# Optimization experiments

Measured on AMD Instinct MI355X. Metric: run time of the kernel, lower is better.

The kernel has to match this reference:

```python
import jax, jax.numpy as jnp
import numpy as np

N = 50000       # num nodes
E = 800000      # num edges (avg degree 16)
D = 128         # in_dim = hidden_dim = out_dim
C = 10          # n_classes
NOISE_STD = 0.1
LN_EPS = 1e-5


def layer_norm(x, g, b):
    mu = jnp.mean(x, axis=-1, keepdims=True)
    var = jnp.mean((x - mu) ** 2, axis=-1, keepdims=True)
    return (x - mu) * jax.lax.rsqrt(var + LN_EPS) * g + b


def gcn_conv(x, W, b, src, dst, dout_isqrt, din_isqrt):
    # DGL GraphConv, norm='both': h = D_in^{-1/2} A (D_out^{-1/2} x W) + b
    h = (x * dout_isqrt[:, None]) @ W              # [N, D] transform first (in>=out)
    agg = jax.ops.segment_sum(h[src], dst, num_segments=x.shape[0])  # SpMM via gather+scatter
    return agg * din_isqrt[:, None] + b


def setup_inputs() -> dict:
    key = jax.random.key(0)
    ks = jax.random.split(key, 16)
    inv = 1.0 / np.sqrt(D)
    return {
        "feat": jax.random.normal(ks[0], (N, D), jnp.float32),
        "noise": jax.random.normal(ks[1], (N, D), jnp.float32),
        "node_mask": jax.random.bernoulli(ks[2], 0.1, (N,)),
        "src": jax.random.randint(ks[3], (E,), 0, N, jnp.int32),
        "dst": jax.random.randint(ks[4], (E,), 0, N, jnp.int32),
        "mask_token": jax.random.normal(ks[5], (D,), jnp.float32) * inv,
        "W0": jax.random.normal(ks[6], (D, D), jnp.float32) * inv,
        "b0": jnp.zeros((D,), jnp.float32),
        "ln0_g": jnp.ones((D,), jnp.float32),
        "ln0_b": jnp.zeros((D,), jnp.float32),
        "W1": jax.random.normal(ks[7], (D, D), jnp.float32) * inv,
        "b1": jnp.zeros((D,), jnp.float32),
        "ln1_g": jnp.ones((D,), jnp.float32),
        "ln1_b": jnp.zeros((D,), jnp.float32),
        "dec_W1": jax.random.normal(ks[8], (D, D), jnp.float32) * inv,
        "dec_b1": jnp.zeros((D,), jnp.float32),
        "dec_W2": jax.random.normal(ks[9], (D, D), jnp.float32) * inv,
        "dec_b2": jnp.zeros((D,), jnp.float32),
        "cls_W": jax.random.normal(ks[10], (D, C), jnp.float32) * inv,
        "cls_b": jnp.zeros((C,), jnp.float32),
    }


def reference(feat, noise, node_mask, src, dst, mask_token,
              W0, b0, ln0_g, ln0_b, W1, b1, ln1_g, ln1_b,
              dec_W1, dec_b1, dec_W2, dec_b2, cls_W, cls_b):
    n = feat.shape[0]
    ones_e = jnp.ones(src.shape, feat.dtype)
    deg_out = jax.ops.segment_sum(ones_e, src, num_segments=n)
    deg_in = jax.ops.segment_sum(ones_e, dst, num_segments=n)
    dout_isqrt = jnp.where(deg_out > 0, jax.lax.rsqrt(jnp.maximum(deg_out, 1.0)), 0.0)
    din_isqrt = jnp.where(deg_in > 0, jax.lax.rsqrt(jnp.maximum(deg_in, 1.0)), 0.0)

    # node masking + noise injection (eval mode: dropout is identity)
    x_masked = jnp.where(node_mask[:, None], mask_token[None, :], feat) + noise * NOISE_STD

    # encoder: layer 0 (conv -> LN -> ReLU), layer 1 (conv -> LN)
    h = gcn_conv(x_masked, W0, b0, src, dst, dout_isqrt, din_isqrt)
    h = jax.nn.relu(layer_norm(h, ln0_g, ln0_b))
    h = gcn_conv(h, W1, b1, src, dst, dout_isqrt, din_isqrt)
    z = layer_norm(h, ln1_g, ln1_b)

    x_recon = jax.nn.relu(z @ dec_W1 + dec_b1) @ dec_W2 + dec_b2
    logits = z @ cls_W + cls_b
    return (x_recon, feat, node_mask, z, logits)
```

## Files before the change

### kernel.cpp

```cpp
#include <hip/hip_runtime.h>
#include <hip/hip_bf16.h>

#define LN_EPS 1e-5f
#define HB 64
#define HSEG 12800
#define NBLK 128
#define BROWS 64
#define WPSTRIDE 17408

typedef __attribute__((ext_vector_type(8))) short short8;
typedef __attribute__((ext_vector_type(4))) float f32x4;

__device__ __forceinline__ unsigned short f2bf(float f) {
    unsigned int u = __float_as_uint(f);
    u += 0x7fffu + ((u >> 16) & 1u);
    return (unsigned short)(u >> 16);
}
__device__ __forceinline__ unsigned int pack2bf(float a, float b) {
    return (unsigned int)f2bf(a) | ((unsigned int)f2bf(b) << 16);
}
__device__ __forceinline__ float bflo(unsigned int v) { return __uint_as_float(v << 16); }
__device__ __forceinline__ float bfhi(unsigned int v) { return __uint_as_float(v & 0xffff0000u); }

__global__ __launch_bounds__(512) void k_hist(const int* __restrict__ src, int* __restrict__ partials,
                                              int N, int E) {
    __shared__ int h[HSEG];
    int chunk = blockIdx.x & (HB - 1);
    int seg = blockIdx.x >> 6;
    int lo = seg * HSEG;
    int len = N - lo;
    if (len > HSEG) len = HSEG;
    if (len <= 0) return;
    for (int i = threadIdx.x; i < len; i += 512) h[i] = 0;
    __syncthreads();
    int per = (E + HB - 1) / HB;
    int e0 = chunk * per, e1 = min(e0 + per, E);
    for (int e = e0 + threadIdx.x; e < e1; e += 512) {
        int s = src[e] - lo;
        if ((unsigned)s < (unsigned)len) atomicAdd(&h[s], 1);
    }
    __syncthreads();
    for (int i = threadIdx.x; i < len; i += 512)
        partials[(size_t)chunk * N + lo + i] = h[i];
}

__global__ __launch_bounds__(256) void k_reduce(const int* __restrict__ partials,
                                                float* __restrict__ doutv, int N) {
    int i = blockIdx.x * 256 + threadIdx.x;
    if (i >= N) return;
    int s = 0;
#pragma unroll
    for (int b = 0; b < HB; ++b) s += partials[(size_t)b * N + i];
    doutv[i] = s > 0 ? 1.0f / sqrtf((float)s) : 0.0f;
}

__global__ __launch_bounds__(256) void k_front(const int* __restrict__ dst, int* __restrict__ counts,
                                               const float* __restrict__ Wa, const float* __restrict__ Wb,
                                               const float* __restrict__ Wc, const float* __restrict__ Wd,
                                               unsigned short* __restrict__ wpack,
                                               const float* __restrict__ feat, const float* __restrict__ noise,
                                               const int* __restrict__ mask, const float* __restrict__ token,
                                               unsigned short* __restrict__ xs, float* __restrict__ feat_out,
                                               float* __restrict__ mask_out,
                                               int nbuck, int E, int n) {
    __shared__ int h[1024];
    int bid = blockIdx.x;
    int tid = threadIdx.x;
    if (bid < NBLK) {
        for (int i = tid; i < nbuck; i += 256) h[i] = 0;
        __syncthreads();
        int per = (E + NBLK - 1) / NBLK;
        int e0 = bid * per, e1 = min(e0 + per, E);
        for (int e = e0 + tid; e < e1; e += 256) atomicAdd(&h[dst[e] >> 6], 1);
        __syncthreads();
        for (int i = tid; i < nbuck; i += 256) counts[(size_t)i * NBLK + bid] = h[i];
        return;
    }
    bid -= NBLK;
    if (bid < 256) {
        int idx = bid * 256 + tid;
        int wsel = idx >> 14;
        int within = idx & 16383;
        const float* W = wsel == 0 ? Wa : wsel == 1 ? Wb : wsel == 2 ? Wc : Wd;
        int c = within >> 7, kk = within & 127;
        wpack[(size_t)wsel * WPSTRIDE + c * 136 + kk] = f2bf(W[kk * 128 + c]);
        return;
    }
    bid -= 256;
    int i = bid * 256 + tid;
    int total = n * 32;
    if (i >= total) return;
    int row = i >> 5, q = i & 31;
    float4 f = ((const float4*)feat)[i];
    float4 nz = ((const float4*)noise)[i];
    bool m = mask[row] != 0;
    float4 b = f;
    if (m) b = ((const float4*)token)[q];
    uint2 p;
    p.x = pack2bf(b.x + 0.1f * nz.x, b.y + 0.1f * nz.y);
    p.y = pack2bf(b.z + 0.1f * nz.z, b.w + 0.1f * nz.w);
    ((uint2*)xs)[i] = p;
    ((float4*)feat_out)[i] = f;
    if (q == 0) mask_out[row] = m ? 1.0f : 0.0f;
}

__global__ __launch_bounds__(128) void k_binB1(const int* __restrict__ counts, int* __restrict__ tot) {
    __shared__ int sm[128];
    int t = threadIdx.x;
    sm[t] = counts[(size_t)blockIdx.x * NBLK + t];
    __syncthreads();
#pragma unroll
    for (int o = 64; o >= 1; o >>= 1) {
        if (t < o) sm[t] += sm[t + o];
        __syncthreads();
    }
    if (t == 0) tot[blockIdx.x] = sm[0];
}

__global__ __launch_bounds__(1024) void k_binB2(const int* __restrict__ tot, int* __restrict__ base,
                                                int nbuck, int E) {
    __shared__ int sm[1024];
    int t = threadIdx.x;
    int v = (t < nbuck) ? tot[t] : 0;
    sm[t] = v;
    __syncthreads();
    for (int o = 1; o < 1024; o <<= 1) {
        int u = (t >= o) ? sm[t - o] : 0;
        __syncthreads();
        sm[t] += u;
        __syncthreads();
    }
    if (t < nbuck) base[t] = sm[t] - v;
    if (t == 0) base[nbuck] = E;
}

__global__ __launch_bounds__(128) void k_binB3(const int* __restrict__ counts, const int* __restrict__ base,
                                               int* __restrict__ offs) {
    __shared__ int sm[128];
    int t = threadIdx.x;
    int v = counts[(size_t)blockIdx.x * NBLK + t];
    sm[t] = v;
    __syncthreads();
    for (int o = 1; o < 128; o <<= 1) {
        int u = (t >= o) ? sm[t - o] : 0;
        __syncthreads();
        sm[t] += u;
        __syncthreads();
    }
    offs[(size_t)blockIdx.x * NBLK + t] = base[blockIdx.x] + sm[t] - v;
}

__global__ __launch_bounds__(256) void k_binC(const int* __restrict__ src, const int* __restrict__ dst,
                                              const int* __restrict__ offs, uint2* __restrict__ binned,
                                              int nbuck, int E) {
    __shared__ int cur[1024];
    for (int i = threadIdx.x; i < nbuck; i += 256) cur[i] = offs[(size_t)i * NBLK + blockIdx.x];
    __syncthreads();
    int per = (E + NBLK - 1) / NBLK;
    int e0 = blockIdx.x * per, e1 = min(e0 + per, E);
    for (int e = e0 + threadIdx.x; e < e1; e += 256) {
        int d = dst[e];
        int p = atomicAdd(&cur[d >> 6], 1);
        binned[p] = make_uint2((unsigned)src[e], (unsigned)d);
    }
}

__global__ __launch_bounds__(256) void k_csr(const uint2* __restrict__ binned, const int* __restrict__ base,
                                             int* __restrict__ row_ptr, int* __restrict__ csr_src, int N) {
    __shared__ int hcnt[BROWS], ccur[BROWS];
    int b = blockIdx.x, t = threadIdx.x;
    int e0 = base[b], e1 = base[b + 1];
    if (t < BROWS) hcnt[t] = 0;
    __syncthreads();
    for (int e = e0 + t; e < e1; e += 256)
        atomicAdd(&hcnt[binned[e].y & (BROWS - 1)], 1);
    __syncthreads();
    if (t < BROWS) {
        int acc = 0;
        for (int r = 0; r < t; ++r) acc += hcnt[r];
        ccur[t] = acc;
        int gw = b * BROWS + t;
        if (gw <= N) row_ptr[gw] = e0 + acc;
    }
    __syncthreads();
    for (int e = e0 + t; e < e1; e += 256) {
        uint2 ed = binned[e];
        int p = atomicAdd(&ccur[ed.y & (BROWS - 1)], 1);
        csr_src[e0 + p] = (int)ed.x;
    }
}

template <int EPI, int OUT_BF16, int DOUT>
__global__ __launch_bounds__(256) void k_gemm_mfma(const unsigned short* __restrict__ A,
                                                   const unsigned short* __restrict__ Wp,
                                                   const float* __restrict__ bias,
                                                   const float* __restrict__ dscale,
                                                   void* __restrict__ Cout, int n) {
    __shared__ uint4 BtV[2176];
    unsigned short* Bt = (unsigned short*)BtV;
    int tid = threadIdx.x;
    const uint4* Wv = (const uint4*)Wp;
    for (int i = tid; i < 2176; i += 256) BtV[i] = Wv[i];
    __syncthreads();

    int wid = tid >> 6, lane = tid & 63;
    int q = lane >> 4, m = lane & 15;
    int r0 = blockIdx.x * 128 + wid * 32;

    f32x4 acc[2][8];
#pragma unroll
    for (int i = 0; i < 2; ++i)
#pragma unroll
        for (int j = 0; j < 8; ++j) acc[i][j] = (f32x4){0.f, 0.f, 0.f, 0.f};

#pragma unroll
    for (int ks = 0; ks < 4; ++ks) {
        int k0 = ks * 32 + q * 8;
        short8 a[2];
#pragma unroll
        for (int i = 0; i < 2; ++i) {
            int row = r0 + i * 16 + m;
            if (row > n - 1) row = n - 1;
            a[i] = *(const short8*)(A + (size_t)row * 128 + k0);
        }
        short8 b[8];
#pragma unroll
        for (int j = 0; j < 8; ++j)
            b[j] = *(const short8*)(&Bt[(j * 16 + m) * 136 + k0]);
#pragma unroll
        for (int i = 0; i < 2; ++i)
#pragma unroll
            for (int j = 0; j < 8; ++j)
                acc[i][j] = __builtin_amdgcn_mfma_f32_16x16x32_bf16(a[i], b[j], acc[i][j], 0, 0, 0);
    }

    float bv[8];
    if (EPI >= 1) {
#pragma unroll
        for (int j = 0; j < 8; ++j) bv[j] = bias[j * 16 + m];
    }

#pragma unroll
    for (int i = 0; i < 2; ++i) {
#pragma unroll
        for (int r = 0; r < 4; ++r) {
            int row = r0 + i * 16 + q * 4 + r;
            if (row < n) {
                float ds = DOUT ? dscale[row] : 1.0f;
#pragma unroll
                for (int j = 0; j < 8; ++j) {
                    float v = acc[i][j][r];
                    if (DOUT) v *= ds;
                    if (EPI >= 1) v += bv[j];
                    if (EPI == 2) v = fmaxf(v, 0.0f);
                    if (OUT_BF16)
                        ((unsigned short*)Cout)[(size_t)row * 128 + j * 16 + m] = f2bf(v);
                    else
                        ((float*)Cout)[(size_t)row * 128 + j * 16 + m] = v;
                }
            }
        }
    }
}

__global__ __launch_bounds__(256) void k_gemm_cls(const unsigned short* __restrict__ A,
                                                  const unsigned short* __restrict__ Wp,
                                                  const float* __restrict__ bias,
                                                  void* __restrict__ Cout,
                                                  const float* __restrict__ cW, const float* __restrict__ cbias,
                                                  float* __restrict__ logits,
                                                  int n, int C, int gb) {
    __shared__ uint4 BtV[2176];
    unsigned short* Bt = (unsigned short*)BtV;
    int tid = threadIdx.x;
    if ((int)blockIdx.x >= gb) {
        int gpos = ((int)blockIdx.x - gb) * 256 + tid;
        int row = gpos >> 4, c = gpos & 15;
        if (row >= n || c >= C) return;
        const unsigned int* zr = (const unsigned int*)(A + (size_t)row * 128);
        float acc = cbias[c];
#pragma unroll 8
        for (int kk = 0; kk < 64; ++kk) {
            unsigned int v = zr[kk];
            acc = fmaf(bflo(v), cW[(2 * kk) * C + c], acc);
            acc = fmaf(bfhi(v), cW[(2 * kk + 1) * C + c], acc);
        }
        logits[(size_t)row * C + c] = acc;
        return;
    }
    const uint4* Wv = (const uint4*)Wp;
    for (int i = tid; i < 2176; i += 256) BtV[i] = Wv[i];
    __syncthreads();

    int wid = tid >> 6, lane = tid & 63;
    int q = lane >> 4, m = lane & 15;
    int r0 = blockIdx.x * 128 + wid * 32;

    f32x4 acc[2][8];
#pragma unroll
    for (int i = 0; i < 2; ++i)
#pragma unroll
        for (int j = 0; j < 8; ++j) acc[i][j] = (f32x4){0.f, 0.f, 0.f, 0.f};

#pragma unroll
    for (int ks = 0; ks < 4; ++ks) {
        int k0 = ks * 32 + q * 8;
        short8 a[2];
#pragma unroll
        for (int i = 0; i < 2; ++i) {
            int row = r0 + i * 16 + m;
            if (row > n - 1) row = n - 1;
            a[i] = *(const short8*)(A + (size_t)row * 128 + k0);
        }
        short8 b[8];
#pragma unroll
        for (int j = 0; j < 8; ++j)
            b[j] = *(const short8*)(&Bt[(j * 16 + m) * 136 + k0]);
#pragma unroll
        for (int i = 0; i < 2; ++i)
#pragma unroll
            for (int j = 0; j < 8; ++j)
                acc[i][j] = __builtin_amdgcn_mfma_f32_16x16x32_bf16(a[i], b[j], acc[i][j], 0, 0, 0);
    }

    float bv[8];
#pragma unroll
    for (int j = 0; j < 8; ++j) bv[j] = bias[j * 16 + m];

#pragma unroll
    for (int i = 0; i < 2; ++i) {
#pragma unroll
        for (int r = 0; r < 4; ++r) {
            int row = r0 + i * 16 + q * 4 + r;
            if (row < n) {
#pragma unroll
                for (int j = 0; j < 8; ++j) {
                    float v = acc[i][j][r] + bv[j];
                    v = fmaxf(v, 0.0f);
                    ((unsigned short*)Cout)[(size_t)row * 128 + j * 16 + m] = f2bf(v);
                }
            }
        }
    }
}

template <int MODE>
__global__ __launch_bounds__(256) void k_agg_ln(const unsigned short* __restrict__ H,
                                                const int* __restrict__ row_ptr,
                                                const int* __restrict__ csr_src,
                                                const float* __restrict__ cb, const float* __restrict__ g,
                                                const float* __restrict__ bt,
                                                float* __restrict__ out_f32, unsigned short* __restrict__ out_bf,
                                                int n) {
    int gw = (blockIdx.x * blockDim.x + threadIdx.x) >> 6;
    int lane = threadIdx.x & 63;
    if (gw >= n) return;
    int beg = row_ptr[gw], end = row_ptr[gw + 1];
    int cnt = end - beg;
    const unsigned int* Hu = (const unsigned int*)H;
    float ax0 = 0.f, ay0 = 0.f, ax1 = 0.f, ay1 = 0.f;
    float ax2 = 0.f, ay2 = 0.f, ax3 = 0.f, ay3 = 0.f;
    for (int c0 = beg; c0 < end; c0 += 64) {
        int m = end - c0;
        if (m > 64) m = 64;
        int myidx = (lane < m) ? csr_src[c0 + lane] : 0;
        int k = 0;
        for (; k + 7 < m; k += 8) {
            int s0 = __shfl(myidx, k + 0), s1 = __shfl(myidx, k + 1);
            int s2 = __shfl(myidx, k + 2), s3 = __shfl(myidx, k + 3);
            int s4 = __shfl(myidx, k + 4), s5 = __shfl(myidx, k + 5);
            int s6 = __shfl(myidx, k + 6), s7 = __shfl(myidx, k + 7);
            unsigned int v0 = Hu[(size_t)s0 * 64 + lane];
            unsigned int v1 = Hu[(size_t)s1 * 64 + lane];
            unsigned int v2 = Hu[(size_t)s2 * 64 + lane];
            unsigned int v3 = Hu[(size_t)s3 * 64 + lane];
            unsigned int v4 = Hu[(size_t)s4 * 64 + lane];
            unsigned int v5 = Hu[(size_t)s5 * 64 + lane];
            unsigned int v6 = Hu[(size_t)s6 * 64 + lane];
            unsigned int v7 = Hu[(size_t)s7 * 64 + lane];
            ax0 += bflo(v0); ay0 += bfhi(v0);
            ax1 += bflo(v1); ay1 += bfhi(v1);
            ax2 += bflo(v2); ay2 += bfhi(v2);
            ax3 += bflo(v3); ay3 += bfhi(v3);
            ax0 += bflo(v4); ay0 += bfhi(v4);
            ax1 += bflo(v5); ay1 += bfhi(v5);
            ax2 += bflo(v6); ay2 += bfhi(v6);
            ax3 += bflo(v7); ay3 += bfhi(v7);
        }
        for (; k < m; ++k) {
            int s0 = __shfl(myidx, k);
            unsigned int v0 = Hu[(size_t)s0 * 64 + lane];
            ax0 += bflo(v0); ay0 += bfhi(v0);
        }
    }
    int d0 = lane * 2;
    float sc = cnt > 0 ? 1.0f / sqrtf((float)cnt) : 0.0f;
    float2 cbv = *(const float2*)(cb + d0);
    float2 x;
    x.x = (ax0 + ax1 + ax2 + ax3) * sc + cbv.x;
    x.y = (ay0 + ay1 + ay2 + ay3) * sc + cbv.y;

    float s = x.x + x.y;
#pragma unroll
    for (int mm = 32; mm >= 1; mm >>= 1) s += __shfl_xor(s, mm, 64);
    float mu = s * (1.0f / 128.0f);
    float dx = x.x - mu, dy = x.y - mu;
    float v = dx * dx + dy * dy;
#pragma unroll
    for (int mm = 32; mm >= 1; mm >>= 1) v += __shfl_xor(v, mm, 64);
    float inv = 1.0f / sqrtf(v * (1.0f / 128.0f) + LN_EPS);
    float2 gv = *(const float2*)(g + d0);
    float2 bv = *(const float2*)(bt + d0);
    float y0 = dx * inv * gv.x + bv.x;
    float y1 = dy * inv * gv.y + bv.y;
    if (MODE == 1) {
        y0 = fmaxf(y0, 0.0f);
        y1 = fmaxf(y1, 0.0f);
    } else {
        *(float2*)(out_f32 + (size_t)gw * 128 + d0) = make_float2(y0, y1);
    }
    ((unsigned int*)out_bf)[(size_t)gw * 64 + lane] = pack2bf(y0, y1);
}

extern "C" void kernel_launch(void* const* d_in, const int* in_sizes, int n_in,
                              void* d_out, int out_size, void* d_ws, size_t ws_size,
                              hipStream_t stream) {
    const float* feat  = (const float*)d_in[0];
    const float* noise = (const float*)d_in[1];
    const int*   nmask = (const int*)d_in[2];
    const int*   src   = (const int*)d_in[3];
    const int*   dst   = (const int*)d_in[4];
    const float* token = (const float*)d_in[5];
    const float* W0    = (const float*)d_in[6];
    const float* b0    = (const float*)d_in[7];
    const float* ln0g  = (const float*)d_in[8];
    const float* ln0b  = (const float*)d_in[9];
    const float* W1    = (const float*)d_in[10];
    const float* b1    = (const float*)d_in[11];
    const float* ln1g  = (const float*)d_in[12];
    const float* ln1b  = (const float*)d_in[13];
    const float* dW1   = (const float*)d_in[14];
    const float* db1   = (const float*)d_in[15];
    const float* dW2   = (const float*)d_in[16];
    const float* db2   = (const float*)d_in[17];
    const float* cW    = (const float*)d_in[18];
    const float* cbias = (const float*)d_in[19];

    const int N = in_sizes[0] / 128;
    const int E = in_sizes[3];
    const int C = in_sizes[19];
    const size_t ND = (size_t)N * 128;
    const int NBUCK = (N + BROWS - 1) / BROWS;
    const int NSEG = (N + HSEG - 1) / HSEG;

    float* out       = (float*)d_out;
    float* out_recon = out;
    float* out_feat  = out + ND;
    float* out_mask  = out + 2 * ND;
    float* out_z     = out + 2 * ND + N;
    float* out_log   = out + 3 * ND + N;

    char* w = (char*)d_ws;
    unsigned short* bufX = (unsigned short*)w; w += ND * 2;
    unsigned short* bufH = (unsigned short*)w; w += ND * 2;
    unsigned short* zbf  = (unsigned short*)w; w += ND * 2;
    unsigned short* wpack = (unsigned short*)w; w += (size_t)4 * WPSTRIDE * 2;
    float* doutv   = (float*)w; w += (size_t)N * 4;
    int* row_ptr   = (int*)w;   w += (size_t)(N + 4) * 4;
    int* csr_src   = (int*)w;   w += (size_t)E * 4;
    int* scratch   = (int*)w;

    int* partials = scratch;
    uint2* binned = (uint2*)scratch;
    int* counts = scratch + (size_t)HB * N;
    int* tot    = counts + (size_t)NBUCK * NBLK;
    int* base   = tot + NBUCK;
    int* offs   = base + NBUCK + 2;

    k_hist<<<HB * NSEG, 512, 0, stream>>>(src, partials, N, E);

    int prep_blocks = (N * 32 + 255) / 256;
    k_front<<<NBLK + 256 + prep_blocks, 256, 0, stream>>>(dst, counts, W0, W1, dW1, dW2, wpack,
                                                          feat, noise, nmask, token,
                                                          bufX, out_feat, out_mask, NBUCK, E, N);

    int nb = (N + 255) / 256;
    k_reduce<<<nb, 256, 0, stream>>>(partials, doutv, N);
    k_binB1<<<NBUCK, 128, 0, stream>>>(counts, tot);
    k_binB2<<<1, 1024, 0, stream>>>(tot, base, NBUCK, E);
    k_binB3<<<NBUCK, 128, 0, stream>>>(counts, base, offs);

    k_binC<<<NBLK, 256, 0, stream>>>(src, dst, offs, binned, NBUCK, E);
    k_csr<<<NBUCK, 256, 0, stream>>>(binned, base, row_ptr, csr_src, N);

    int gb = (N + 127) / 128;
    int rb = (N * 64 + 255) / 256;

    k_gemm_mfma<0, 1, 1><<<gb, 256, 0, stream>>>(bufX, wpack + 0 * WPSTRIDE, nullptr, doutv, bufH, N);
    k_agg_ln<1><<<rb, 256, 0, stream>>>(bufH, row_ptr, csr_src, b0, ln0g, ln0b, nullptr, bufX, N);

    k_gemm_mfma<0, 1, 1><<<gb, 256, 0, stream>>>(bufX, wpack + 1 * WPSTRIDE, nullptr, doutv, bufH, N);
    k_agg_ln<0><<<rb, 256, 0, stream>>>(bufH, row_ptr, csr_src, b1, ln1g, ln1b, out_z, zbf, N);

    int cls_blocks = (N * 16 + 255) / 256;
    k_gemm_cls<<<gb + cls_blocks, 256, 0, stream>>>(zbf, wpack + 2 * WPSTRIDE, db1, bufX,
                                                    cW, cbias, out_log, N, C, gb);

    k_gemm_mfma<1, 0, 0><<<gb, 256, 0, stream>>>(bufX, wpack + 3 * WPSTRIDE, db2, nullptr, out_recon, N);
}
```

Measured before the change: 212.1 us.

## Fuse decoder GEMMs via LDS and split edge gather across half-waves

The two decoder GEMMs become one kernel: the ReLU'd hidden tile is staged in LDS as bf16 and fed straight into the second MFMA GEMM, so the intermediate no longer goes through global memory. The classifier head moves to its own kernel. The aggregation kernel now has each half-wave gather a different neighbor row with 8-byte loads and combines the halves with a cross-half shuffle, which doubles the edges in flight per wave. The costs are doubled LDS per decoder block, which may lower occupancy, and the extra shuffle reduction step.

```diff
diff --git a/kernel.cpp b/kernel.cpp
--- a/kernel.cpp
+++ b/kernel.cpp
@@ -263,34 +263,19 @@
     }
 }
 
-__global__ __launch_bounds__(256) void k_gemm_cls(const unsigned short* __restrict__ A,
-                                                  const unsigned short* __restrict__ Wp,
-                                                  const float* __restrict__ bias,
-                                                  void* __restrict__ Cout,
-                                                  const float* __restrict__ cW, const float* __restrict__ cbias,
-                                                  float* __restrict__ logits,
-                                                  int n, int C, int gb) {
-    __shared__ uint4 BtV[2176];
-    unsigned short* Bt = (unsigned short*)BtV;
+__global__ __launch_bounds__(256) void k_dec(const unsigned short* __restrict__ A,
+                                             const unsigned short* __restrict__ Wp1, const float* __restrict__ bias1,
+                                             const unsigned short* __restrict__ Wp2, const float* __restrict__ bias2,
+                                             float* __restrict__ Cout, int n) {
+    __shared__ uint4 W1V[2176];
+    __shared__ uint4 W2V[2176];
     int tid = threadIdx.x;
-    if ((int)blockIdx.x >= gb) {
-        int gpos = ((int)blockIdx.x - gb) * 256 + tid;
-        int row = gpos >> 4, c = gpos & 15;
-        if (row >= n || c >= C) return;
-        const unsigned int* zr = (const unsigned int*)(A + (size_t)row * 128);
-        float acc = cbias[c];
-#pragma unroll 8
-        for (int kk = 0; kk < 64; ++kk) {
-            unsigned int v = zr[kk];
-            acc = fmaf(bflo(v), cW[(2 * kk) * C + c], acc);
-            acc = fmaf(bfhi(v), cW[(2 * kk + 1) * C + c], acc);
-        }
-        logits[(size_t)row * C + c] = acc;
-        return;
-    }
-    const uint4* Wv = (const uint4*)Wp;
-    for (int i = tid; i < 2176; i += 256) BtV[i] = Wv[i];
-    __syncthreads();
+    const uint4* w1 = (const uint4*)Wp1;
+    const uint4* w2 = (const uint4*)Wp2;
+    for (int i = tid; i < 2176; i += 256) { W1V[i] = w1[i]; W2V[i] = w2[i]; }
+    __syncthreads();
+    unsigned short* W1s = (unsigned short*)W1V;
+    unsigned short* W2s = (unsigned short*)W2V;
 
     int wid = tid >> 6, lane = tid & 63;
     int q = lane >> 4, m = lane & 15;
@@ -301,7 +286,6 @@
     for (int i = 0; i < 2; ++i)
 #pragma unroll
         for (int j = 0; j < 8; ++j) acc[i][j] = (f32x4){0.f, 0.f, 0.f, 0.f};
-
 #pragma unroll
     for (int ks = 0; ks < 4; ++ks) {
         int k0 = ks * 32 + q * 8;
@@ -315,33 +299,66 @@
         short8 b[8];
 #pragma unroll
         for (int j = 0; j < 8; ++j)
-            b[j] = *(const short8*)(&Bt[(j * 16 + m) * 136 + k0]);
+            b[j] = *(const short8*)(&W1s[(j * 16 + m) * 136 + k0]);
 #pragma unroll
         for (int i = 0; i < 2; ++i)
 #pragma unroll
             for (int j = 0; j < 8; ++j)
                 acc[i][j] = __builtin_amdgcn_mfma_f32_16x16x32_bf16(a[i], b[j], acc[i][j], 0, 0, 0);
     }
-
     float bv[8];
 #pragma unroll
-    for (int j = 0; j < 8; ++j) bv[j] = bias[j * 16 + m];
-
-#pragma unroll
-    for (int i = 0; i < 2; ++i) {
+    for (int j = 0; j < 8; ++j) bv[j] = bias1[j * 16 + m];
+
+    __syncthreads();
+    unsigned short* T = W1s;
+#pragma unroll
+    for (int i = 0; i < 2; ++i)
+#pragma unroll
+        for (int r = 0; r < 4; ++r) {
+            int lrow = wid * 32 + i * 16 + q * 4 + r;
+#pragma unroll
+            for (int j = 0; j < 8; ++j) {
+                float v = acc[i][j][r] + bv[j];
+                T[lrow * 136 + j * 16 + m] = f2bf(fmaxf(v, 0.0f));
+            }
+        }
+    __syncthreads();
+
+#pragma unroll
+    for (int i = 0; i < 2; ++i)
+#pragma unroll
+        for (int j = 0; j < 8; ++j) acc[i][j] = (f32x4){0.f, 0.f, 0.f, 0.f};
+#pragma unroll
+    for (int ks = 0; ks < 4; ++ks) {
+        int k0 = ks * 32 + q * 8;
+        short8 a[2];
+#pragma unroll
+        for (int i = 0; i < 2; ++i)
+            a[i] = *(const short8*)(&T[(wid * 32 + i * 16 + m) * 136 + k0]);
+        short8 b[8];
+#pragma unroll
+        for (int j = 0; j < 8; ++j)
+            b[j] = *(const short8*)(&W2s[(j * 16 + m) * 136 + k0]);
+#pragma unroll
+        for (int i = 0; i < 2; ++i)
+#pragma unroll
+            for (int j = 0; j < 8; ++j)
+                acc[i][j] = __builtin_amdgcn_mfma_f32_16x16x32_bf16(a[i], b[j], acc[i][j], 0, 0, 0);
+    }
+#pragma unroll
+    for (int j = 0; j < 8; ++j) bv[j] = bias2[j * 16 + m];
+#pragma unroll
+    for (int i = 0; i < 2; ++i)
 #pragma unroll
         for (int r = 0; r < 4; ++r) {
             int row = r0 + i * 16 + q * 4 + r;
             if (row < n) {
 #pragma unroll
-                for (int j = 0; j < 8; ++j) {
-                    float v = acc[i][j][r] + bv[j];
-                    v = fmaxf(v, 0.0f);
-                    ((unsigned short*)Cout)[(size_t)row * 128 + j * 16 + m] = f2bf(v);
-                }
-            }
-        }
-    }
+                for (int j = 0; j < 8; ++j)
+                    Cout[(size_t)row * 128 + j * 16 + m] = acc[i][j][r] + bv[j];
+            }
+        }
 }
 
 template <int MODE>
@@ -357,69 +374,110 @@
     if (gw >= n) return;
     int beg = row_ptr[gw], end = row_ptr[gw + 1];
     int cnt = end - beg;
-    const unsigned int* Hu = (const unsigned int*)H;
-    float ax0 = 0.f, ay0 = 0.f, ax1 = 0.f, ay1 = 0.f;
-    float ax2 = 0.f, ay2 = 0.f, ax3 = 0.f, ay3 = 0.f;
+    const uint2* H2 = (const uint2*)H;
+    int half = lane >> 5;
+    int hl = lane & 31;
+    float a0 = 0.f, a1 = 0.f, a2 = 0.f, a3 = 0.f;
     for (int c0 = beg; c0 < end; c0 += 64) {
         int m = end - c0;
         if (m > 64) m = 64;
         int myidx = (lane < m) ? csr_src[c0 + lane] : 0;
         int k = 0;
+        for (; k + 15 < m; k += 16) {
+            uint2 v[8];
+#pragma unroll
+            for (int p = 0; p < 8; ++p) {
+                int s = __shfl(myidx, k + 2 * p + half);
+                v[p] = H2[(size_t)s * 32 + hl];
+            }
+#pragma unroll
+            for (int p = 0; p < 8; ++p) {
+                a0 += bflo(v[p].x); a1 += bfhi(v[p].x);
+                a2 += bflo(v[p].y); a3 += bfhi(v[p].y);
+            }
+        }
         for (; k + 7 < m; k += 8) {
-            int s0 = __shfl(myidx, k + 0), s1 = __shfl(myidx, k + 1);
-            int s2 = __shfl(myidx, k + 2), s3 = __shfl(myidx, k + 3);
-            int s4 = __shfl(myidx, k + 4), s5 = __shfl(myidx, k + 5);
-            int s6 = __shfl(myidx, k + 6), s7 = __shfl(myidx, k + 7);
-            unsigned int v0 = Hu[(size_t)s0 * 64 + lane];
-            unsigned int v1 = Hu[(size_t)s1 * 64 + lane];
-            unsigned int v2 = Hu[(size_t)s2 * 64 + lane];
-            unsigned int v3 = Hu[(size_t)s3 * 64 + lane];
-            unsigned int v4 = Hu[(size_t)s4 * 64 + lane];
-            unsigned int v5 = Hu[(size_t)s5 * 64 + lane];
-            unsigned int v6 = Hu[(size_t)s6 * 64 + lane];
-            unsigned int v7 = Hu[(size_t)s7 * 64 + lane];
-            ax0 += bflo(v0); ay0 += bfhi(v0);
-            ax1 += bflo(v1); ay1 += bfhi(v1);
-            ax2 += bflo(v2); ay2 += bfhi(v2);
-            ax3 += bflo(v3); ay3 += bfhi(v3);
-            ax0 += bflo(v4); ay0 += bfhi(v4);
-            ax1 += bflo(v5); ay1 += bfhi(v5);
-            ax2 += bflo(v6); ay2 += bfhi(v6);
-            ax3 += bflo(v7); ay3 += bfhi(v7);
-        }
-        for (; k < m; ++k) {
-            int s0 = __shfl(myidx, k);
-            unsigned int v0 = Hu[(size_t)s0 * 64 + lane];
-            ax0 += bflo(v0); ay0 += bfhi(v0);
-        }
-    }
-    int d0 = lane * 2;
+            uint2 v[4];
+#pragma unroll
+            for (int p = 0; p < 4; ++p) {
+                int s = __shfl(myidx, k + 2 * p + half);
+                v[p] = H2[(size_t)s * 32 + hl];
+            }
+#pragma unroll
+            for (int p = 0; p < 4; ++p) {
+                a0 += bflo(v[p].x); a1 += bfhi(v[p].x);
+                a2 += bflo(v[p].y); a3 += bfhi(v[p].y);
+            }
+        }
+        for (; k < m; k += 2) {
+            int e = k + half;
+            int s = __shfl(myidx, (e < m) ? e : k);
+            uint2 vv = H2[(size_t)s * 32 + hl];
+            if (e < m) {
+                a0 += bflo(vv.x); a1 += bfhi(vv.x);
+                a2 += bflo(vv.y); a3 += bfhi(vv.y);
+            }
+        }
+    }
+    a0 += __shfl_xor(a0, 32, 64);
+    a1 += __shfl_xor(a1, 32, 64);
+    a2 += __shfl_xor(a2, 32, 64);
+    a3 += __shfl_xor(a3, 32, 64);
+
+    int d0 = hl * 4;
     float sc = cnt > 0 ? 1.0f / sqrtf((float)cnt) : 0.0f;
-    float2 cbv = *(const float2*)(cb + d0);
-    float2 x;
-    x.x = (ax0 + ax1 + ax2 + ax3) * sc + cbv.x;
-    x.y = (ay0 + ay1 + ay2 + ay3) * sc + cbv.y;
-
-    float s = x.x + x.y;
-#pragma unroll
-    for (int mm = 32; mm >= 1; mm >>= 1) s += __shfl_xor(s, mm, 64);
+    float4 cbv = *(const float4*)(cb + d0);
+    float x0 = a0 * sc + cbv.x;
+    float x1 = a1 * sc + cbv.y;
+    float x2 = a2 * sc + cbv.z;
+    float x3 = a3 * sc + cbv.w;
+
+    float s = x0 + x1 + x2 + x3;
+#pragma unroll
+    for (int mm = 16; mm >= 1; mm >>= 1) s += __shfl_xor(s, mm, 64);
     float mu = s * (1.0f / 128.0f);
-    float dx = x.x - mu, dy = x.y - mu;
-    float v = dx * dx + dy * dy;
-#pragma unroll
-    for (int mm = 32; mm >= 1; mm >>= 1) v += __shfl_xor(v, mm, 64);
+    float dx0 = x0 - mu, dx1 = x1 - mu, dx2 = x2 - mu, dx3 = x3 - mu;
+    float v = dx0 * dx0 + dx1 * dx1 + dx2 * dx2 + dx3 * dx3;
+#pragma unroll
+    for (int mm = 16; mm >= 1; mm >>= 1) v += __shfl_xor(v, mm, 64);
     float inv = 1.0f / sqrtf(v * (1.0f / 128.0f) + LN_EPS);
-    float2 gv = *(const float2*)(g + d0);
-    float2 bv = *(const float2*)(bt + d0);
-    float y0 = dx * inv * gv.x + bv.x;
-    float y1 = dy * inv * gv.y + bv.y;
+    float4 gv = *(const float4*)(g + d0);
+    float4 bvv = *(const float4*)(bt + d0);
+    float y0 = dx0 * inv * gv.x + bvv.x;
+    float y1 = dx1 * inv * gv.y + bvv.y;
+    float y2 = dx2 * inv * gv.z + bvv.z;
+    float y3 = dx3 * inv * gv.w + bvv.w;
     if (MODE == 1) {
-        y0 = fmaxf(y0, 0.0f);
-        y1 = fmaxf(y1, 0.0f);
-    } else {
-        *(float2*)(out_f32 + (size_t)gw * 128 + d0) = make_float2(y0, y1);
-    }
-    ((unsigned int*)out_bf)[(size_t)gw * 64 + lane] = pack2bf(y0, y1);
+        y0 = fmaxf(y0, 0.0f); y1 = fmaxf(y1, 0.0f);
+        y2 = fmaxf(y2, 0.0f); y3 = fmaxf(y3, 0.0f);
+    }
+    if (half == 0) {
+        if (MODE == 0) {
+            float4 z4 = make_float4(y0, y1, y2, y3);
+            *(float4*)(out_f32 + (size_t)gw * 128 + d0) = z4;
+        }
+        uint2 pk;
+        pk.x = pack2bf(y0, y1);
+        pk.y = pack2bf(y2, y3);
+        ((uint2*)out_bf)[(size_t)gw * 32 + hl] = pk;
+    }
+}
+
+__global__ __launch_bounds__(256) void k_cls(const unsigned short* __restrict__ Z, const float* __restrict__ W,
+                                             const float* __restrict__ b, float* __restrict__ out,
+                                             int n, int C) {
+    int gpos = blockIdx.x * blockDim.x + threadIdx.x;
+    int row = gpos >> 4, c = gpos & 15;
+    if (row >= n || c >= C) return;
+    const unsigned int* zr = (const unsigned int*)(Z + (size_t)row * 128);
+    float acc = b[c];
+#pragma unroll 8
+    for (int kk = 0; kk < 64; ++kk) {
+        unsigned int v = zr[kk];
+        acc = fmaf(bflo(v), W[(2 * kk) * C + c], acc);
+        acc = fmaf(bfhi(v), W[(2 * kk + 1) * C + c], acc);
+    }
+    out[(size_t)row * C + c] = acc;
 }
 
 extern "C" void kernel_launch(void* const* d_in, const int* in_sizes, int n_in,
@@ -502,9 +560,7 @@
     k_gemm_mfma<0, 1, 1><<<gb, 256, 0, stream>>>(bufX, wpack + 1 * WPSTRIDE, nullptr, doutv, bufH, N);
     k_agg_ln<0><<<rb, 256, 0, stream>>>(bufH, row_ptr, csr_src, b1, ln1g, ln1b, out_z, zbf, N);
 
-    int cls_blocks = (N * 16 + 255) / 256;
-    k_gemm_cls<<<gb + cls_blocks, 256, 0, stream>>>(zbf, wpack + 2 * WPSTRIDE, db1, bufX,
-                                                    cW, cbias, out_log, N, C, gb);
-
-    k_gemm_mfma<1, 0, 0><<<gb, 256, 0, stream>>>(bufX, wpack + 3 * WPSTRIDE, db2, nullptr, out_recon, N);
-}
+    k_cls<<<(N * 16 + 255) / 256, 256, 0, stream>>>(zbf, cW, cbias, out_log, N, C);
+
+    k_dec<<<gb, 256, 0, stream>>>(zbf, wpack + 2 * WPSTRIDE, db1, wpack + 3 * WPSTRIDE, db2, out_recon, N);
+}
```

New measurement: 199.5 us. 6.0% less time.
